# Kernel optimization log

Measured on AMD Instinct MI355X. Metric: run time of the kernel, lower is better.

Reference implementation:

```python
import jax, jax.numpy as jnp
from jax import lax
import numpy as np

H = W = 32          # feature map size (1024px image / stride 32)
A = 9               # 3 scales x 3 ratios
IOU_THR = 0.5
DN = ('NCHW', 'OIHW', 'NCHW')


def _base_anchors():
    scales = [8.0, 16.0, 32.0]
    ratios = [0.5, 1.0, 2.0]
    rows = []
    for s in scales:
        for r in ratios:
            w = s * np.sqrt(r)
            h = s / np.sqrt(r)
            rows.append([-w / 2, -h / 2, w / 2, h / 2])
    return jnp.asarray(np.array(rows, dtype=np.float32))  # [A,4]


def setup_inputs() -> dict:
    key = jax.random.key(0)
    ks = jax.random.split(key, 4)
    x = jax.random.normal(ks[0], (1, 2048, H, W), jnp.float32)
    # small weight scale keeps exp(dw) in a sane range, like a trained RPN
    conv_w = jax.random.normal(ks[1], (512, 2048, 3, 3), jnp.float32) * 0.01
    conv_b = jnp.zeros((512,), jnp.float32)
    cls_w = jax.random.normal(ks[2], (2 * A, 512, 1, 1), jnp.float32) * 0.01
    cls_b = jnp.zeros((2 * A,), jnp.float32)
    bbox_w = jax.random.normal(ks[3], (4 * A, 512, 1, 1), jnp.float32) * 0.01
    bbox_b = jnp.zeros((4 * A,), jnp.float32)
    return {"x": x, "conv_w": conv_w, "conv_b": conv_b,
            "cls_w": cls_w, "cls_b": cls_b, "bbox_w": bbox_w, "bbox_b": bbox_b}


def _conv(x, w, b, pad):
    y = lax.conv_general_dilated(x, w, (1, 1), pad, dimension_numbers=DN)
    return y + b[None, :, None, None]


def _pairwise_iou(boxes):
    # boxes: [N,4] (x1,y1,x2,y2)
    area = (boxes[:, 2] - boxes[:, 0]) * (boxes[:, 3] - boxes[:, 1])
    lt = jnp.maximum(boxes[:, None, :2], boxes[None, :, :2])
    rb = jnp.minimum(boxes[:, None, 2:], boxes[None, :, 2:])
    wh = jnp.clip(rb - lt, 0.0)
    inter = wh[..., 0] * wh[..., 1]
    union = area[:, None] + area[None, :] - inter
    return inter / jnp.maximum(union, 1e-9)


def _nms_keep(boxes_sorted):
    # boxes sorted by descending score; sequential greedy suppression
    n = boxes_sorted.shape[0]
    iou = _pairwise_iou(boxes_sorted)  # [N,N]
    idx = jnp.arange(n)
    def body(i, keep):
        sup = (iou[i] > IOU_THR) & (idx > i) & keep[i]
        return keep & ~sup
    return lax.fori_loop(0, n, body, jnp.ones((n,), bool))


def _rpn_forward(x, conv_w, conv_b, cls_w, cls_b, bbox_w, bbox_b):
    feat = jax.nn.relu(_conv(x, conv_w, conv_b, 'SAME'))            # [1,512,H,W]
    obj = _conv(feat, cls_w, cls_b, 'VALID')                        # [1,18,H,W]
    deltas = _conv(feat, bbox_w, bbox_b, 'VALID')                   # [1,36,H,W]

    # softmax over the 2 classes (torch view(B,2,-1): first 9 channels = class 0)
    probs = jax.nn.softmax(obj[0].reshape(2, -1), axis=0)[1]        # [A*H*W] anchor-major
    scores = probs.reshape(A, H, W).transpose(1, 2, 0).reshape(-1)  # (pos, anchor) order

    # bbox channel layout: channel = a*4 + coord (0::4 slicing in torch)
    d = deltas[0].reshape(A, 4, H, W).transpose(2, 3, 0, 1).reshape(-1, 4)  # [N,4]

    anchors = jnp.tile(_base_anchors(), (H * W, 1))                 # [N,4], pos*9+a
    aw = anchors[:, 2] - anchors[:, 0]
    ah = anchors[:, 3] - anchors[:, 1]
    cx = anchors[:, 0] + 0.5 * aw
    cy = anchors[:, 1] + 0.5 * ah
    px = cx + d[:, 0] * aw
    py = cy + d[:, 1] * ah
    pw = jnp.exp(d[:, 2]) * aw
    ph = jnp.exp(d[:, 3]) * ah
    boxes = jnp.stack([px - 0.5 * pw, py - 0.5 * ph,
                       px + 0.5 * pw, py + 0.5 * ph], axis=1)       # [N,4]

    order = jnp.argsort(-scores)
    boxes_s = boxes[order]
    scores_s = scores[order]
    keep = _nms_keep(boxes_s)
    final_boxes = jnp.where(keep[:, None], boxes_s, 0.0)
    final_scores = jnp.where(keep, scores_s, 0.0)
    return final_boxes, final_scores


def reference(x, conv_w, conv_b, cls_w, cls_b, bbox_w, bbox_b):
    return _rpn_forward(x, conv_w, conv_b, cls_w, cls_b, bbox_w, bbox_b)
```

## Files before the change

### kernel.cpp

```cpp
#include <hip/hip_runtime.h>
#include <cstdint>
#include <cmath>

#define HH 32
#define WW 32
#define NPX 1024
#define CIN 2048
#define CMID 512
#define NA 9
#define NBOX 9216
#define NWRD 144

typedef double f64x4 __attribute__((ext_vector_type(4)));

#if defined(__HIP_DEVICE_COMPILE__)
#if __has_builtin(__builtin_amdgcn_mfma_f64_16x16x4f64)
#define MFMA64(a, b, c) __builtin_amdgcn_mfma_f64_16x16x4f64((a), (b), (c), 0, 0, 0)
#elif __has_builtin(__builtin_amdgcn_mfma_f64_16x16x4_f64)
#define MFMA64(a, b, c) __builtin_amdgcn_mfma_f64_16x16x4_f64((a), (b), (c), 0, 0, 0)
#endif
#endif

__global__ void k_probe(int* __restrict__ flag) {
#ifdef MFMA64
  const int lane = threadIdx.x & 63;
  const int q = lane >> 4, n16 = lane & 15;
  f64x4 z = {0.0, 0.0, 0.0, 0.0};
  f64x4 d1 = MFMA64((double)(n16 + 1), (n16 == 0) ? 1.0 : 0.0, z);
  f64x4 d2 = MFMA64(1.0, (double)(n16 + 1), z);
  bool ok0 = true, ok1 = true, ok2 = true, ok3 = true;
#pragma unroll
  for (int r = 0; r < 4; ++r) {
    const double rc = (double)(4 * q + r + 1);
    const double rs = (double)(q + 4 * r + 1);
    const double p1 = d1[r], p2 = d2[r];
    const double colv = 4.0 * (double)(n16 + 1);
    ok0 &= (p1 == ((n16 == 0) ? 4.0 * rc : 0.0)) && (p2 == colv);
    ok1 &= (p1 == ((n16 == 0) ? 4.0 * rs : 0.0)) && (p2 == colv);
    ok2 &= (p1 == ((4 * q + r == 0) ? colv : 0.0)) && (p2 == 4.0 * rc);
    ok3 &= (p1 == ((q + 4 * r == 0) ? colv : 0.0)) && (p2 == 4.0 * rs);
  }
  const unsigned long long full = ~0ull;
  int f = 0;
  if (__ballot(ok0) == full) f = 1;
  else if (__ballot(ok1) == full) f = 2;
  else if (__ballot(ok2) == full) f = 3;
  else if (__ballot(ok3) == full) f = 4;
  if (threadIdx.x == 0) *flag = f;
#else
  if (threadIdx.x == 0) *flag = 0;
#endif
}

__global__ __launch_bounds__(256) void k_conv3x3_mfma(
    const float* __restrict__ x, const float* __restrict__ wgt,
    double* __restrict__ partial, int chunk, const int* __restrict__ flag) {
#ifdef MFMA64
  const int f = *flag;
  if (f == 0) return;
  const bool swp = (f >= 3);
  const bool contig = (f == 1) || (f == 3);

  __shared__ double xs[2][8 * 153];
  __shared__ float  wsm[2][72 * 73];
  const int tid = threadIdx.x;
  const int pxt = blockIdx.x;
  const int oct = blockIdx.y;
  const int cz  = blockIdx.z;
  const int h0  = pxt * 2;
  const int oc0 = oct * 64;
  const int cbase = cz * chunk;

  const int wv   = tid >> 6;
  const int lane = tid & 63;
  const int q    = lane >> 4;
  const int n16  = lane & 15;

  f64x4 acc[4];
#pragma unroll
  for (int t = 0; t < 4; ++t) acc[t] = (f64x4){0.0, 0.0, 0.0, 0.0};

  float xreg[5];
  float wreg[18];

#define LOAD_STAGE(C0)                                                         \
  {                                                                            \
    _Pragma("unroll")                                                          \
    for (int k = 0; k < 5; ++k) {                                              \
      const int idx = tid + k * 256;                                           \
      float v = 0.f;                                                           \
      if (idx < 1152) {                                                        \
        const int cc = idx / 144, rem = idx - cc * 144;                        \
        const int r = rem / 36, lcol = rem - r * 36;                           \
        const int grow = h0 - 1 + r, gcol = lcol - 1;                          \
        if ((unsigned)grow < 32u && (unsigned)gcol < 32u)                      \
          v = x[((size_t)((C0) + cc) << 10) + (grow << 5) + gcol];             \
      }                                                                        \
      xreg[k] = v;                                                             \
    }                                                                          \
    _Pragma("unroll")                                                          \
    for (int k = 0; k < 18; ++k) {                                             \
      const int idx = tid + k * 256;                                           \
      const int oc_l = idx / 72, rem = idx - oc_l * 72;                        \
      wreg[k] = wgt[(size_t)(oc0 + oc_l) * 18432 + (size_t)(C0) * 9 + rem];    \
    }                                                                          \
  }

#define WRITE_STAGE(P)                                                         \
  {                                                                            \
    _Pragma("unroll")                                                          \
    for (int k = 0; k < 5; ++k) {                                              \
      const int idx = tid + k * 256;                                           \
      if (idx < 1152) {                                                        \
        const int cc = idx / 144, rem = idx - cc * 144;                        \
        const int r = rem / 36, lcol = rem - r * 36;                           \
        xs[P][cc * 153 + r * 38 + lcol] = (double)xreg[k];                     \
      }                                                                        \
    }                                                                          \
    _Pragma("unroll")                                                          \
    for (int k = 0; k < 18; ++k) {                                             \
      const int idx = tid + k * 256;                                           \
      const int oc_l = idx / 72, rem = idx - oc_l * 72;                        \
      const int cc = rem / 9, tap = rem - cc * 9;                              \
      wsm[P][(tap * 8 + cc) * 73 + oc_l] = wreg[k];                            \
    }                                                                          \
  }

  const int nst = chunk >> 3;
  LOAD_STAGE(cbase)
  WRITE_STAGE(0)
  __syncthreads();

  for (int s = 0; s < nst; ++s) {
    const int p = s & 1;
    if (s + 1 < nst) LOAD_STAGE(cbase + (s + 1) * 8)
    __builtin_amdgcn_sched_barrier(0);

    const double* xb = &xs[p][q * 153 + n16];
    const float*  wb = &wsm[p][q * 73 + (wv << 4) + n16];

#define CONV_INNER(SWPV)                                                       \
    _Pragma("unroll")                                                          \
    for (int tap = 0; tap < 9; ++tap) {                                        \
      const int dy = tap / 3, dx = tap - 3 * (tap / 3);                        \
      _Pragma("unroll")                                                        \
      for (int ksg = 0; ksg < 2; ++ksg) {                                      \
        const double av = (double)wb[(tap * 8 + ksg * 4) * 73];                \
        const double* xq = xb + ksg * 612;                     \
        _Pragma("unroll")                                                      \
        for (int t = 0; t < 4; ++t) {                                          \
          const double bv = xq[((t >> 1) + dy) * 38 + (t & 1) * 16 + dx];      \
          if (SWPV) acc[t] = MFMA64(bv, av, acc[t]);                           \
          else      acc[t] = MFMA64(av, bv, acc[t]);                           \
        }                                                                      \
      }                                                                        \
    }

    if (swp) { CONV_INNER(true) } else { CONV_INNER(false) }
#undef CONV_INNER

    if (s + 1 < nst) {
      WRITE_STAGE(p ^ 1)
      __syncthreads();
    }
  }
#undef LOAD_STAGE
#undef WRITE_STAGE
  double* out = partial + (size_t)cz * (CMID * NPX);
#pragma unroll
  for (int t = 0; t < 4; ++t) {
    const int px = ((h0 + (t >> 1)) << 5) + ((t & 1) << 4) + n16;
#pragma unroll
    for (int j = 0; j < 4; ++j) {
      const int row = contig ? ((q << 2) + j) : (q + (j << 2));
      const int oc = oc0 + (wv << 4) + row;
      out[(size_t)oc * NPX + px] = acc[t][j];
    }
  }
#endif
}

__global__ __launch_bounds__(256) void k_conv3x3_valu(
    const float* __restrict__ x, const float* __restrict__ wgt,
    double* __restrict__ partial, int chunk, const int* __restrict__ flag) {
  if (*flag != 0) return;
  __shared__ double xs[8][4][36];
  __shared__ double ws_s[8 * 9 * 66];
  const int tid = threadIdx.x;
  const int pxt = blockIdx.x;
  const int oct = blockIdx.y;
  const int cz  = blockIdx.z;
  const int h0  = pxt * 2;
  const int oc0 = oct * 64;
  const int cbase = cz * chunk;

  const int g   = tid & 15;
  const int ty  = tid >> 4;
  const int r_p = g >> 3;
  const int gc  = (g & 7) * 4;

  double acc[4][4];
#pragma unroll
  for (int a = 0; a < 4; ++a)
#pragma unroll
    for (int b = 0; b < 4; ++b) acc[a][b] = 0.0;

  const int stages = chunk >> 3;
  for (int s = 0; s < stages; ++s) {
    const int c0 = cbase + s * 8;
    __syncthreads();
    for (int idx = tid; idx < 1152; idx += 256) {
      int cc = idx / 144, rem = idx - cc * 144;
      int r = rem / 36, lcol = rem - r * 36;
      int grow = h0 - 1 + r, gcol = lcol - 1;
      float v = 0.f;
      if ((unsigned)grow < 32u && (unsigned)gcol < 32u)
        v = x[((size_t)(c0 + cc) << 10) + (grow << 5) + gcol];
      xs[cc][r][lcol] = (double)v;
    }
    for (int idx = tid; idx < 4608; idx += 256) {
      int oc_l = idx / 72, rem = idx - oc_l * 72;
      int cc = rem / 9, t = rem - cc * 9;
      ws_s[(cc * 9 + t) * 66 + oc_l] =
          (double)wgt[(size_t)(oc0 + oc_l) * 18432 + (size_t)(c0 + cc) * 9 + t];
    }
    __syncthreads();
    for (int cc = 0; cc < 8; ++cc) {
      double xr[3][8];
#pragma unroll
      for (int dy = 0; dy < 3; ++dy) {
        const double* xp = &xs[cc][r_p + dy][gc];
#pragma unroll
        for (int k = 0; k < 8; ++k) xr[dy][k] = xp[k];
      }
#pragma unroll
      for (int t = 0; t < 9; ++t) {
        const int dy = t / 3, dx = t - dy * 3;
        const double* wp = &ws_s[(cc * 9 + t) * 66 + ty * 4];
        const double w0 = wp[0], w1 = wp[1], w2 = wp[2], w3 = wp[3];
#pragma unroll
        for (int i = 0; i < 4; ++i) {
          const double xv = xr[dy][i + dx];
          acc[0][i] += w0 * xv;
          acc[1][i] += w1 * xv;
          acc[2][i] += w2 * xv;
          acc[3][i] += w3 * xv;
        }
      }
    }
  }
  const int pxg = (h0 + r_p) * 32 + gc;
  double* out = partial + (size_t)cz * (CMID * NPX);
#pragma unroll
  for (int j = 0; j < 4; ++j)
#pragma unroll
    for (int i = 0; i < 4; ++i)
      out[(size_t)(oc0 + ty * 4 + j) * NPX + pxg + i] = acc[j][i];
}

__global__ void k_reduce(const double* __restrict__ partial,
                         const float* __restrict__ bias,
                         double* __restrict__ feat, int S) {
  int idx = blockIdx.x * 256 + threadIdx.x;
  double s = (double)bias[idx >> 10];
  for (int z = 0; z < S; ++z) s += partial[(size_t)z * (CMID * NPX) + idx];
  feat[idx] = fmax(s, 0.0);
}

__global__ void k_1x1(const double* __restrict__ feat,
                      const float* __restrict__ cls_w, const float* __restrict__ cls_b,
                      const float* __restrict__ bbox_w, const float* __restrict__ bbox_b,
                      double* __restrict__ logits) {
  int px = blockIdx.x * 256 + threadIdx.x;
  int ch = blockIdx.y;
  const float* wv;
  float bias;
  if (ch < 18) { wv = cls_w + (size_t)ch * 512; bias = cls_b[ch]; }
  else         { wv = bbox_w + (size_t)(ch - 18) * 512; bias = bbox_b[ch - 18]; }
  double acc = 0.0;
  for (int c = 0; c < 512; ++c)
    acc += feat[((size_t)c << 10) + px] * (double)wv[c];
  logits[((size_t)ch << 10) + px] = acc + (double)bias;
}

__global__ void k_score_box(const double* __restrict__ logits,
                            double* __restrict__ scores, double* __restrict__ boxes) {
  int i = blockIdx.x * 256 + threadIdx.x;
  int pos = i / 9, a = i - pos * 9;
  const double* obj = logits;
  const double* dl  = logits + 18 * NPX;
  double l0 = obj[a * NPX + pos], l1 = obj[(9 + a) * NPX + pos];
  double delta = l1 - l0;
  scores[i] = 1.0 / (1.0 + exp(-delta));
  double d0 = dl[(a * 4 + 0) * NPX + pos], d1 = dl[(a * 4 + 1) * NPX + pos];
  double d2 = dl[(a * 4 + 2) * NPX + pos], d3 = dl[(a * 4 + 3) * NPX + pos];
  const double s_arr[3] = {8.0, 16.0, 32.0};
  const double r_arr[3] = {0.5, 1.0, 2.0};
  double sA = s_arr[a / 3], rA = r_arr[a % 3];
  double aw = (double)(float)(sA * sqrt(rA));
  double ah = (double)(float)(sA / sqrt(rA));
  double px_ = d0 * aw, py_ = d1 * ah;
  double pw = exp(d2) * aw, ph = exp(d3) * ah;
  boxes[i * 4 + 0] = px_ - 0.5 * pw;
  boxes[i * 4 + 1] = py_ - 0.5 * ph;
  boxes[i * 4 + 2] = px_ + 0.5 * pw;
  boxes[i * 4 + 3] = py_ + 0.5 * ph;
}

__global__ void k_rank_count(const double* __restrict__ scores, int* __restrict__ rank) {
  __shared__ double sj[256];
  int i  = blockIdx.x * 256 + threadIdx.x;
  int jb = blockIdx.y * 256;
  sj[threadIdx.x] = scores[jb + threadIdx.x];
  __syncthreads();
  double si = scores[i];
  int cnt = 0;
  for (int t = 0; t < 256; ++t) {
    double s = sj[t];
    int j = jb + t;
    cnt += (int)((s > si) || (s == si && j < i));
  }
  if (cnt) atomicAdd(&rank[i], cnt);
}

__global__ void k_scatter(const double* __restrict__ scores, const double* __restrict__ boxes,
                          const int* __restrict__ rank,
                          double* __restrict__ scores_s, double* __restrict__ boxes_s) {
  int i = blockIdx.x * 256 + threadIdx.x;
  int r = rank[i];
  scores_s[r] = scores[i];
  boxes_s[r * 4 + 0] = boxes[i * 4 + 0];
  boxes_s[r * 4 + 1] = boxes[i * 4 + 1];
  boxes_s[r * 4 + 2] = boxes[i * 4 + 2];
  boxes_s[r * 4 + 3] = boxes[i * 4 + 3];
}

__global__ void k_mask(const double* __restrict__ boxes_s, unsigned long long* __restrict__ mask) {
  __shared__ double jb[256][4];
  __shared__ double ib[64][4];
  const int tid = threadIdx.x;
  const int j0 = blockIdx.x * 256;
  const int i0 = blockIdx.y * 64;
  for (int idx = tid; idx < 1024; idx += 256) jb[idx >> 2][idx & 3] = boxes_s[j0 * 4 + idx];
  for (int idx = tid; idx < 256; idx += 256) ib[idx >> 2][idx & 3] = boxes_s[i0 * 4 + idx];
  __syncthreads();
  const int il = tid >> 2;
  const int i  = i0 + il;
  const int wq = blockIdx.x * 4 + (tid & 3);
  const int jlb = (tid & 3) * 64;
  unsigned long long m = 0ull;
  if (wq * 64 + 63 > i) {
    double ix1 = ib[il][0], iy1 = ib[il][1], ix2 = ib[il][2], iy2 = ib[il][3];
    double iarea = (ix2 - ix1) * (iy2 - iy1);
    for (int b = 0; b < 64; ++b) {
      int j = wq * 64 + b;
      double jx1 = jb[jlb + b][0], jy1 = jb[jlb + b][1];
      double jx2 = jb[jlb + b][2], jy2 = jb[jlb + b][3];
      double xx1 = fmax(ix1, jx1), yy1 = fmax(iy1, jy1);
      double xx2 = fmin(ix2, jx2), yy2 = fmin(iy2, jy2);
      double iw = fmax(xx2 - xx1, 0.0), ih = fmax(yy2 - yy1, 0.0);
      double inter = iw * ih;
      double jarea = (jx2 - jx1) * (jy2 - jy1);
      double uni = fmax(iarea + jarea - inter, 1e-9);
      bool sup = inter > 0.5 * uni;
      if (sup && j > i) m |= (1ull << b);
    }
  }
  mask[(size_t)i * NWRD + wq] = m;
}

__global__ void k_nms_scan(const unsigned long long* __restrict__ mask,
                           int* __restrict__ keep) {
  const int l = threadIdx.x & 63;
  unsigned long long r0 = 0ull, r1 = 0ull, r2 = (l < 16) ? 0ull : ~0ull;
  const int w0 = l, w1 = l + 64, w2 = l + 128;
  int prev = -1;
  while (true) {
    int cand = 1 << 30;
    unsigned long long b;
    b = ~r0;
    if (w0 * 64 <= prev) b = (w0 * 64 + 63 <= prev) ? 0ull : (b & (~0ull << (prev + 1 - w0 * 64)));
    if (b) cand = w0 * 64 + __ffsll((long long)b) - 1;
    b = ~r1;
    if (w1 * 64 <= prev) b = (w1 * 64 + 63 <= prev) ? 0ull : (b & (~0ull << (prev + 1 - w1 * 64)));
    if (b) { int c = w1 * 64 + __ffsll((long long)b) - 1; cand = c < cand ? c : cand; }
    b = ~r2;
    if (w2 * 64 <= prev) b = (w2 * 64 + 63 <= prev) ? 0ull : (b & (~0ull << (prev + 1 - w2 * 64)));
    if (b) { int c = w2 * 64 + __ffsll((long long)b) - 1; cand = c < cand ? c : cand; }
#pragma unroll
    for (int off = 32; off; off >>= 1) {
      int o = __shfl_xor(cand, off);
      cand = o < cand ? o : cand;
    }
    if (cand >= NBOX) break;
    const int i = cand;
    if (l == 0) keep[i] = 1;
    r0 |= mask[(size_t)i * NWRD + w0];
    r1 |= mask[(size_t)i * NWRD + w1];
    if (l < 16) r2 |= mask[(size_t)i * NWRD + w2];
    prev = i;
  }
}

__global__ void k_finalize(const double* __restrict__ boxes_s, const double* __restrict__ scores_s,
                           const int* __restrict__ keep, float* __restrict__ out) {
  int r = blockIdx.x * 256 + threadIdx.x;
  int k = keep[r];
  out[r * 4 + 0] = k ? (float)boxes_s[r * 4 + 0] : 0.f;
  out[r * 4 + 1] = k ? (float)boxes_s[r * 4 + 1] : 0.f;
  out[r * 4 + 2] = k ? (float)boxes_s[r * 4 + 2] : 0.f;
  out[r * 4 + 3] = k ? (float)boxes_s[r * 4 + 3] : 0.f;
  out[NBOX * 4 + r] = k ? (float)scores_s[r] : 0.f;
}

static inline size_t alignup(size_t v, size_t a) { return (v + a - 1) & ~(a - 1); }

extern "C" void kernel_launch(void* const* d_in, const int* in_sizes, int n_in,
                              void* d_out, int out_size, void* d_ws, size_t ws_size,
                              hipStream_t stream) {
  const float* x      = (const float*)d_in[0];
  const float* conv_w = (const float*)d_in[1];
  const float* conv_b = (const float*)d_in[2];
  const float* cls_w  = (const float*)d_in[3];
  const float* cls_b  = (const float*)d_in[4];
  const float* bbox_w = (const float*)d_in[5];
  const float* bbox_b = (const float*)d_in[6];
  float* out = (float*)d_out;

  char* ws = (char*)d_ws;
  size_t off = 0;
  int* flag = (int*)(ws + off); off = alignup(off + 256, 256);
  unsigned long long* mask = (unsigned long long*)(ws + off); off = alignup(off + (size_t)NBOX * NWRD * 8, 256);
  double* feat     = (double*)(ws + off); off = alignup(off + (size_t)CMID * NPX * 8, 256);
  double* logits   = (double*)(ws + off); off = alignup(off + (size_t)54 * NPX * 8, 256);
  double* scores   = (double*)(ws + off); off = alignup(off + (size_t)NBOX * 8, 256);
  double* boxes    = (double*)(ws + off); off = alignup(off + (size_t)NBOX * 32, 256);
  double* scores_s = (double*)(ws + off); off = alignup(off + (size_t)NBOX * 8, 256);
  double* boxes_s  = (double*)(ws + off); off = alignup(off + (size_t)NBOX * 32, 256);
  int*   rank      = (int*)(ws + off);    off = alignup(off + (size_t)NBOX * 4, 256);
  int*   keep      = (int*)(ws + off);    off = alignup(off + (size_t)NBOX * 4, 256);
  size_t fixed = off;

  int S = 8;
  while (S > 1 && fixed + (size_t)S * CMID * NPX * 8 > ws_size) S >>= 1;
  double* partial = (double*)(ws + fixed);

  const int chunk = CIN / S;

  hipLaunchKernelGGL(k_probe, dim3(1), dim3(64), 0, stream, flag);
  hipLaunchKernelGGL(k_conv3x3_mfma, dim3(16, 8, S), dim3(256), 0, stream,
                     x, conv_w, partial, chunk, flag);
  hipLaunchKernelGGL(k_conv3x3_valu, dim3(16, 8, S), dim3(256), 0, stream,
                     x, conv_w, partial, chunk, flag);
  hipLaunchKernelGGL(k_reduce, dim3((CMID * NPX) / 256), dim3(256), 0, stream,
                     partial, conv_b, feat, S);
  hipLaunchKernelGGL(k_1x1, dim3(4, 54), dim3(256), 0, stream,
                     feat, cls_w, cls_b, bbox_w, bbox_b, logits);
  hipLaunchKernelGGL(k_score_box, dim3(NBOX / 256), dim3(256), 0, stream,
                     logits, scores, boxes);
  hipMemsetAsync(rank, 0, (size_t)NBOX * 4, stream);
  hipMemsetAsync(keep, 0, (size_t)NBOX * 4, stream);
  hipLaunchKernelGGL(k_rank_count, dim3(36, 36), dim3(256), 0, stream, scores, rank);
  hipLaunchKernelGGL(k_scatter, dim3(NBOX / 256), dim3(256), 0, stream,
                     scores, boxes, rank, scores_s, boxes_s);
  hipLaunchKernelGGL(k_mask, dim3(36, 144), dim3(256), 0, stream, boxes_s, mask);
  hipLaunchKernelGGL(k_nms_scan, dim3(1), dim3(64), 0, stream, mask, keep);
  hipLaunchKernelGGL(k_finalize, dim3(NBOX / 256), dim3(256), 0, stream,
                     boxes_s, scores_s, keep, out);
}
```

Measured before the change: 631.5 us.

## Load conv weights directly into LDS and batch 1x1 channels per block

```diff
diff --git a/kernel.cpp b/kernel.cpp
--- a/kernel.cpp
+++ b/kernel.cpp
@@ -18,6 +18,9 @@
 #define MFMA64(a, b, c) __builtin_amdgcn_mfma_f64_16x16x4f64((a), (b), (c), 0, 0, 0)
 #elif __has_builtin(__builtin_amdgcn_mfma_f64_16x16x4_f64)
 #define MFMA64(a, b, c) __builtin_amdgcn_mfma_f64_16x16x4_f64((a), (b), (c), 0, 0, 0)
+#endif
+#if __has_builtin(__builtin_amdgcn_global_load_lds)
+#define HAVE_GLL 1
 #endif
 #endif
 
@@ -52,7 +55,7 @@
 #endif
 }
 
-__global__ __launch_bounds__(256) void k_conv3x3_mfma(
+__global__ __launch_bounds__(256, 2) void k_conv3x3_mfma(
     const float* __restrict__ x, const float* __restrict__ wgt,
     double* __restrict__ partial, int chunk, const int* __restrict__ flag) {
 #ifdef MFMA64
@@ -62,7 +65,7 @@
   const bool contig = (f == 1) || (f == 3);
 
   __shared__ double xs[2][8 * 153];
-  __shared__ float  wsm[2][72 * 73];
+  __shared__ float  wsm[2][4608];
   const int tid = threadIdx.x;
   const int pxt = blockIdx.x;
   const int oct = blockIdx.y;
@@ -81,63 +84,86 @@
   for (int t = 0; t < 4; ++t) acc[t] = (f64x4){0.0, 0.0, 0.0, 0.0};
 
   float xreg[5];
+
+#ifdef HAVE_GLL
+  int wsrc[5];
+#pragma unroll
+  for (int m = 0; m < 5; ++m) {
+    const int k = wv + 4 * m;
+    const int fidx = k * 256 + lane * 4;
+    const int oc_l = fidx / 72;
+    const int rem  = fidx - oc_l * 72;
+    wsrc[m] = (oc0 + oc_l) * 18432 + rem;
+  }
+#define WISSUE(P, C0)                                                          \
+  _Pragma("unroll")                                                            \
+  for (int m = 0; m < 5; ++m) {                                                \
+    const int k = wv + 4 * m;                                                  \
+    if (k < 18) {                                                              \
+      __builtin_amdgcn_global_load_lds(                                        \
+          (const __attribute__((address_space(1))) void*)(wgt + (size_t)wsrc[m] + (size_t)(C0) * 9), \
+          (__attribute__((address_space(3))) void*)(&wsm[P][k * 256]),         \
+          16, 0, 0);                                                           \
+    }                                                                          \
+  }
+#define WCOMMIT(P)
+#else
   float wreg[18];
-
-#define LOAD_STAGE(C0)                                                         \
-  {                                                                            \
-    _Pragma("unroll")                                                          \
-    for (int k = 0; k < 5; ++k) {                                              \
-      const int idx = tid + k * 256;                                           \
-      float v = 0.f;                                                           \
-      if (idx < 1152) {                                                        \
-        const int cc = idx / 144, rem = idx - cc * 144;                        \
-        const int r = rem / 36, lcol = rem - r * 36;                           \
-        const int grow = h0 - 1 + r, gcol = lcol - 1;                          \
-        if ((unsigned)grow < 32u && (unsigned)gcol < 32u)                      \
-          v = x[((size_t)((C0) + cc) << 10) + (grow << 5) + gcol];             \
-      }                                                                        \
-      xreg[k] = v;                                                             \
+#define WISSUE(P, C0)                                                          \
+  _Pragma("unroll")                                                            \
+  for (int k = 0; k < 18; ++k) {                                               \
+    const int idx = tid + k * 256;                                             \
+    const int oc_l = idx / 72, rem = idx - oc_l * 72;                          \
+    wreg[k] = wgt[(size_t)(oc0 + oc_l) * 18432 + (size_t)(C0) * 9 + rem];      \
+  }
+#define WCOMMIT(P)                                                             \
+  _Pragma("unroll")                                                            \
+  for (int k = 0; k < 18; ++k) wsm[P][tid + k * 256] = wreg[k];
+#endif
+
+#define XLOAD(C0)                                                              \
+  _Pragma("unroll")                                                            \
+  for (int k = 0; k < 5; ++k) {                                                \
+    const int idx = tid + k * 256;                                             \
+    float v = 0.f;                                                             \
+    if (idx < 1152) {                                                          \
+      const int cc = idx / 144, rem = idx - cc * 144;                          \
+      const int r = rem / 36, lcol = rem - r * 36;                             \
+      const int grow = h0 - 1 + r, gcol = lcol - 1;                            \
+      if ((unsigned)grow < 32u && (unsigned)gcol < 32u)                        \
+        v = x[((size_t)((C0) + cc) << 10) + (grow << 5) + gcol];               \
     }                                                                          \
-    _Pragma("unroll")                                                          \
-    for (int k = 0; k < 18; ++k) {                                             \
-      const int idx = tid + k * 256;                                           \
-      const int oc_l = idx / 72, rem = idx - oc_l * 72;                        \
-      wreg[k] = wgt[(size_t)(oc0 + oc_l) * 18432 + (size_t)(C0) * 9 + rem];    \
+    xreg[k] = v;                                                               \
+  }
+
+#define XWRITE(P)                                                              \
+  _Pragma("unroll")                                                            \
+  for (int k = 0; k < 5; ++k) {                                                \
+    const int idx = tid + k * 256;                                             \
+    if (idx < 1152) {                                                          \
+      const int cc = idx / 144, rem = idx - cc * 144;                          \
+      const int r = rem / 36, lcol = rem - r * 36;                             \
+      xs[P][cc * 153 + r * 38 + lcol] = (double)xreg[k];                       \
     }                                                                          \
   }
 
-#define WRITE_STAGE(P)                                                         \
-  {                                                                            \
-    _Pragma("unroll")                                                          \
-    for (int k = 0; k < 5; ++k) {                                              \
-      const int idx = tid + k * 256;                                           \
-      if (idx < 1152) {                                                        \
-        const int cc = idx / 144, rem = idx - cc * 144;                        \
-        const int r = rem / 36, lcol = rem - r * 36;                           \
-        xs[P][cc * 153 + r * 38 + lcol] = (double)xreg[k];                     \
-      }                                                                        \
-    }                                                                          \
-    _Pragma("unroll")                                                          \
-    for (int k = 0; k < 18; ++k) {                                             \
-      const int idx = tid + k * 256;                                           \
-      const int oc_l = idx / 72, rem = idx - oc_l * 72;                        \
-      const int cc = rem / 9, tap = rem - cc * 9;                              \
-      wsm[P][(tap * 8 + cc) * 73 + oc_l] = wreg[k];                            \
-    }                                                                          \
-  }
-
   const int nst = chunk >> 3;
-  LOAD_STAGE(cbase)
-  WRITE_STAGE(0)
+  WISSUE(0, cbase)
+  XLOAD(cbase)
+  XWRITE(0)
+  WCOMMIT(0)
   __syncthreads();
 
   for (int s = 0; s < nst; ++s) {
     const int p = s & 1;
-    if (s + 1 < nst) LOAD_STAGE(cbase + (s + 1) * 8)
+    if (s + 1 < nst) {
+      WISSUE(p ^ 1, cbase + (s + 1) * 8)
+      XLOAD(cbase + (s + 1) * 8)
+    }
     __builtin_amdgcn_sched_barrier(0);
 
-    const double* xb = &xs[p][q * 153 + n16];
-    const float*  wb = &wsm[p][q * 73 + (wv << 4) + n16];
+    const double* xb  = &xs[p][q * 153 + n16];
+    const float*  wbq = &wsm[p][((wv << 4) + n16) * 72 + q * 9];
 
 #define CONV_INNER(SWPV)                                                       \
     _Pragma("unroll")                                                          \
@@ -145,7 +171,7 @@
       const int dy = tap / 3, dx = tap - 3 * (tap / 3);                        \
       _Pragma("unroll")                                                        \
       for (int ksg = 0; ksg < 2; ++ksg) {                                      \
-        const double av = (double)wb[(tap * 8 + ksg * 4) * 73];                \
+        const double av = (double)wbq[ksg * 36 + tap];                         \
         const double* xq = xb + ksg * 612;                     \
         _Pragma("unroll")                                                      \
         for (int t = 0; t < 4; ++t) {                                          \
@@ -160,12 +186,15 @@
 #undef CONV_INNER
 
     if (s + 1 < nst) {
-      WRITE_STAGE(p ^ 1)
+      XWRITE(p ^ 1)
+      WCOMMIT(p ^ 1)
       __syncthreads();
     }
   }
-#undef LOAD_STAGE
-#undef WRITE_STAGE
+#undef WISSUE
+#undef WCOMMIT
+#undef XLOAD
+#undef XWRITE
   double* out = partial + (size_t)cz * (CMID * NPX);
 #pragma unroll
   for (int t = 0; t < 4; ++t) {
@@ -267,20 +296,36 @@
   feat[idx] = fmax(s, 0.0);
 }
 
-__global__ void k_1x1(const double* __restrict__ feat,
-                      const float* __restrict__ cls_w, const float* __restrict__ cls_b,
-                      const float* __restrict__ bbox_w, const float* __restrict__ bbox_b,
-                      double* __restrict__ logits) {
-  int px = blockIdx.x * 256 + threadIdx.x;
-  int ch = blockIdx.y;
-  const float* wv;
-  float bias;
-  if (ch < 18) { wv = cls_w + (size_t)ch * 512; bias = cls_b[ch]; }
-  else         { wv = bbox_w + (size_t)(ch - 18) * 512; bias = bbox_b[ch - 18]; }
-  double acc = 0.0;
-  for (int c = 0; c < 512; ++c)
-    acc += feat[((size_t)c << 10) + px] * (double)wv[c];
-  logits[((size_t)ch << 10) + px] = acc + (double)bias;
+__global__ __launch_bounds__(256) void k_1x1(
+    const double* __restrict__ feat,
+    const float* __restrict__ cls_w, const float* __restrict__ cls_b,
+    const float* __restrict__ bbox_w, const float* __restrict__ bbox_b,
+    double* __restrict__ logits) {
+  __shared__ float wsh[9 * 512];
+  const int px = blockIdx.x * 256 + threadIdx.x;
+  const int cg = blockIdx.y;
+  for (int idx = threadIdx.x; idx < 9 * 512; idx += 256) {
+    int j = idx >> 9, c = idx & 511;
+    int ch = cg * 9 + j;
+    wsh[idx] = (ch < 18) ? cls_w[(size_t)ch * 512 + c]
+                         : bbox_w[(size_t)(ch - 18) * 512 + c];
+  }
+  __syncthreads();
+  double acc[9];
+#pragma unroll
+  for (int j = 0; j < 9; ++j) acc[j] = 0.0;
+  for (int c = 0; c < 512; ++c) {
+    const double fv = feat[((size_t)c << 10) + px];
+#pragma unroll
+    for (int j = 0; j < 9; ++j)
+      acc[j] += fv * (double)wsh[(j << 9) + c];
+  }
+#pragma unroll
+  for (int j = 0; j < 9; ++j) {
+    const int ch = cg * 9 + j;
+    const float bias = (ch < 18) ? cls_b[ch] : bbox_b[ch - 18];
+    logits[((size_t)ch << 10) + px] = acc[j] + (double)bias;
+  }
 }
 
 __global__ void k_score_box(const double* __restrict__ logits,
@@ -454,7 +499,7 @@
                      x, conv_w, partial, chunk, flag);
   hipLaunchKernelGGL(k_reduce, dim3((CMID * NPX) / 256), dim3(256), 0, stream,
                      partial, conv_b, feat, S);
-  hipLaunchKernelGGL(k_1x1, dim3(4, 54), dim3(256), 0, stream,
+  hipLaunchKernelGGL(k_1x1, dim3(4, 6), dim3(256), 0, stream,
                      feat, cls_w, cls_b, bbox_w, bbox_b, logits);
   hipLaunchKernelGGL(k_score_box, dim3(NBOX / 256), dim3(256), 0, stream,
                      logits, scores, boxes);
```

Result: no change. 621.9 us (-1.5%).
